# Performance work log

Hardware: AMD Instinct MI355X
Metric: run time of the kernel (lower is better)

The kernel has to match this reference:

```python
import jax, jax.numpy as jnp
import numpy as np

B, T, C, H = 2, 2048, 1024, 16
N = C // H
TM_DIM, TD_DIM = 32, 64
EPS = 1e-5 * 8 ** 2  # GroupNorm eps from the module


def setup_inputs() -> dict:
    key = jax.random.key(0)
    ks = jax.random.split(key, 16)
    nrm = lambda k, shp, s: jax.random.normal(k, shp, dtype=jnp.float32) * s
    uni = lambda k, shp, a: jax.random.uniform(k, shp, jnp.float32, -a, a)
    ddd = (jnp.arange(C, dtype=jnp.float32) / C).reshape(1, 1, C)
    return {
        "x": nrm(ks[0], (B, T, C), 1.0),
        "time_maa_x": 1.0 - ddd ** 0.5,
        "time_maa_w": 1.0 - ddd ** 0.5,
        "time_maa_k": 1.0 - ddd ** 0.5,
        "time_maa_v": 1.0 - (ddd ** 0.5 + 0.15),
        "time_maa_r": 1.0 - ddd ** 0.25,
        "time_maa_g": 1.0 - ddd ** 0.25,
        "time_maa_w1": uni(ks[1], (C, 5 * TM_DIM), 1e-4),
        "time_maa_w2": uni(ks[2], (5, TM_DIM, C), 1e-4),
        "time_decay": jnp.linspace(-6.0, -1.0, C).astype(jnp.float32).reshape(1, 1, C),
        "time_decay_w1": uni(ks[3], (C, TD_DIM), 1e-4),
        "time_decay_w2": uni(ks[4], (TD_DIM, C), 1e-4),
        "time_faaaa": nrm(ks[5], (H, N), 0.1),
        "W_r": nrm(ks[6], (C, C), C ** -0.5),
        "W_k": nrm(ks[7], (C, C), C ** -0.5),
        "W_v": nrm(ks[8], (C, C), C ** -0.5),
        "W_g": nrm(ks[9], (C, C), C ** -0.5),
        "W_o": nrm(ks[10], (C, C), C ** -0.5),
        "ln_w": jnp.ones((C,), jnp.float32),
        "ln_b": jnp.zeros((C,), jnp.float32),
    }


def _forward(x, tmx, tmw, tmk, tmv, tmr, tmg, maa_w1, maa_w2, tdecay, td_w1,
             td_w2, u, Wr, Wk, Wv, Wg, Wo, ln_w, ln_b):
    Bq, Tq, Cq = x.shape
    # time_shift: x[t-1] with zero at t=0
    xx = jnp.concatenate([jnp.zeros_like(x[:, :1]), x[:, :-1]], axis=1) - x
    xxx = x + xx * tmx
    t5 = jnp.tanh(xxx @ maa_w1).reshape(Bq, Tq, 5, TM_DIM)
    m = jnp.einsum('btfe,fec->fbtc', t5, maa_w2)  # [5,B,T,C] data-dependent mix
    xw = x + xx * (tmw + m[0])
    xk = x + xx * (tmk + m[1])
    xv = x + xx * (tmv + m[2])
    xr = x + xx * (tmr + m[3])
    xg = x + xx * (tmg + m[4])
    r = xr @ Wr
    k = xk @ Wk
    v = xv @ Wv
    g = jax.nn.silu(xg @ Wg)
    w = tdecay + jnp.tanh(xw @ td_w1) @ td_w2          # [B,T,C] log-log decay
    decay = jnp.exp(-jnp.exp(w))                        # in (0,1)
    to_tbhn = lambda a: a.reshape(Bq, Tq, H, N).transpose(1, 0, 2, 3)
    rT, kT, vT, dT = (to_tbhn(a) for a in (r, k, v, decay))

    def step(S, inp):  # S: [B,H,N,N] (key_dim i, value_dim j)
        r_t, k_t, v_t, d_t = inp
        kv = k_t[..., :, None] * v_t[..., None, :]
        y = jnp.einsum('bhi,bhij->bhj', r_t, S + u[None, :, :, None] * kv)
        return d_t[..., None] * S + kv, y

    S0 = jnp.zeros((Bq, H, N, N), x.dtype)
    _, ys = jax.lax.scan(step, S0, (rT, kT, vT, dT))
    y = ys.transpose(1, 0, 2, 3).reshape(Bq, Tq, Cq)
    # GroupNorm with H groups over channels
    yh = y.reshape(Bq, Tq, H, N)
    mu = yh.mean(-1, keepdims=True)
    var = yh.var(-1, keepdims=True)
    yn = (yh - mu) / jnp.sqrt(var + EPS)
    yn = (yn * ln_w.reshape(H, N) + ln_b.reshape(H, N)).reshape(Bq, Tq, Cq)
    return (yn * g) @ Wo


def reference(x, time_maa_x, time_maa_w, time_maa_k, time_maa_v, time_maa_r,
              time_maa_g, time_maa_w1, time_maa_w2, time_decay, time_decay_w1,
              time_decay_w2, time_faaaa, W_r, W_k, W_v, W_g, W_o, ln_w, ln_b):
    return _forward(x, time_maa_x, time_maa_w, time_maa_k, time_maa_v,
                    time_maa_r, time_maa_g, time_maa_w1, time_maa_w2,
                    time_decay, time_decay_w1, time_decay_w2, time_faaaa,
                    W_r, W_k, W_v, W_g, W_o, ln_w, ln_b)
```

## Files before the change

### kernel.cpp

```cpp
#include <hip/hip_runtime.h>
#include <hip/hip_bf16.h>
#include <cstdint>
#include <cstddef>

#define B_ 2
#define T_ 2048
#define C_ 1024
#define H_ 16
#define NCH 32
#define CHL 64

typedef unsigned short ushort_t;
typedef __bf16 bf16x8 __attribute__((ext_vector_type(8)));
typedef float f32x4 __attribute__((ext_vector_type(4)));

__device__ __forceinline__ ushort_t f2bf(float f) {
  union { float f; uint32_t u; } x; x.f = f;
  uint32_t r = x.u + 0x7fffu + ((x.u >> 16) & 1u);
  return (ushort_t)(r >> 16);
}
__device__ __forceinline__ float bf2f(ushort_t h) {
  union { uint32_t u; float f; } x; x.u = (uint32_t)h << 16; return x.f;
}

__device__ __forceinline__ void gload16(const void* g, void* l) {
  __builtin_amdgcn_global_load_lds(
      (const __attribute__((address_space(1))) void*)g,
      (__attribute__((address_space(3))) void*)l, 16, 0, 0);
}

__device__ __forceinline__ void stb(ushort_t* tile, int row, int col, ushort_t v) {
  *(ushort_t*)((char*)tile + row * 128 + ((col * 2) ^ ((row & 7) << 4))) = v;
}
__device__ __forceinline__ bf16x8 ldb(const ushort_t* tile, int row, int kbyte) {
  return *(const bf16x8*)((const char*)tile + row * 128 + (kbyte ^ ((row & 7) << 4)));
}

struct TDesc { const float* src; ushort_t* dst; int R, Cc, Cpad; };
struct TArgs { TDesc d[9]; };

__global__ __launch_bounds__(256) void transpose_cvt(TArgs args) {
  TDesc D = args.d[blockIdx.z];
  int c0 = blockIdx.x * 32, r0 = blockIdx.y * 32;
  if (c0 >= D.Cpad || r0 >= D.R) return;
  __shared__ float tile[32][33];
  int tx = threadIdx.x & 31, ty = threadIdx.x >> 5;
#pragma unroll
  for (int i = 0; i < 32; i += 8) {
    int r = r0 + ty + i, c = c0 + tx;
    tile[ty + i][tx] = (r < D.R && c < D.Cc) ? D.src[(size_t)r * D.Cc + c] : 0.f;
  }
  __syncthreads();
#pragma unroll
  for (int i = 0; i < 32; i += 8) {
    int c = c0 + ty + i, r = r0 + tx;
    if (c < D.Cpad && r < D.R) D.dst[(size_t)c * D.R + r] = f2bf(tile[tx][ty + i]);
  }
}

__global__ __launch_bounds__(256) void prep_kernel(
    const float* __restrict__ x, const float* __restrict__ tmx,
    float* __restrict__ xx, ushort_t* __restrict__ xxx) {
  size_t idx = ((size_t)blockIdx.x * 256 + threadIdx.x) * 4;
  int tt = (int)((idx >> 10) & (T_ - 1));
  int c = (int)(idx & (C_ - 1));
  float4 xv = *(const float4*)&x[idx];
  float4 xp;
  if (tt == 0) { xp.x = xp.y = xp.z = xp.w = 0.f; }
  else xp = *(const float4*)&x[idx - C_];
  float4 tm = *(const float4*)&tmx[c];
  float4 d;
  d.x = xp.x - xv.x; d.y = xp.y - xv.y; d.z = xp.z - xv.z; d.w = xp.w - xv.w;
  *(float4*)&xx[idx] = d;
  xxx[idx + 0] = f2bf(xv.x + d.x * tm.x);
  xxx[idx + 1] = f2bf(xv.y + d.y * tm.y);
  xxx[idx + 2] = f2bf(xv.z + d.z * tm.z);
  xxx[idx + 3] = f2bf(xv.w + d.w * tm.w);
}

template <int EPI>
__global__ __launch_bounds__(256) void gemm_bt(
    const ushort_t* __restrict__ A, int lda,
    const ushort_t* __restrict__ Bt, int ldb,
    void* __restrict__ Cp, int ldc, int K,
    const float* __restrict__ aux2) {
  __shared__ ushort_t sA[128 * 32];
  __shared__ ushort_t sB[128 * 32];
  const int t = threadIdx.x;
  const int l = t & 63;
  const int w = t >> 6;
  const int wm = w >> 1, wn = w & 1;
  const int m0 = blockIdx.x * 128, n0 = blockIdx.y * 128;
  const int lr = l & 15;
  const int lk = (l >> 4) * 8;

  f32x4 acc[4][4] = {};

  for (int kt = 0; kt < K; kt += 32) {
    __syncthreads();
#pragma unroll
    for (int it = 0; it < 2; ++it) {
      int cbase = it * 256 + w * 64;
      int ca = cbase + l;
      int row = ca >> 2, kc = ca & 3;
      gload16(A + (size_t)(m0 + row) * lda + kt + kc * 8, (char*)sA + (size_t)cbase * 16);
      gload16(Bt + (size_t)(n0 + row) * ldb + kt + kc * 8, (char*)sB + (size_t)cbase * 16);
    }
    __syncthreads();
    bf16x8 af[4], bfr[4];
#pragma unroll
    for (int mi = 0; mi < 4; ++mi)
      af[mi] = *(const bf16x8*)&sA[(wm * 64 + mi * 16 + lr) * 32 + lk];
#pragma unroll
    for (int ni = 0; ni < 4; ++ni)
      bfr[ni] = *(const bf16x8*)&sB[(wn * 64 + ni * 16 + lr) * 32 + lk];
#pragma unroll
    for (int mi = 0; mi < 4; ++mi)
#pragma unroll
      for (int ni = 0; ni < 4; ++ni)
        acc[mi][ni] = __builtin_amdgcn_mfma_f32_16x16x32_bf16(af[mi], bfr[ni], acc[mi][ni], 0, 0, 0);
  }
#pragma unroll
  for (int mi = 0; mi < 4; ++mi) {
#pragma unroll
    for (int ni = 0; ni < 4; ++ni) {
      int col = n0 + wn * 64 + ni * 16 + lr;
#pragma unroll
      for (int r = 0; r < 4; ++r) {
        int row = m0 + wm * 64 + mi * 16 + (l >> 4) * 4 + r;
        float v = acc[mi][ni][r];
        size_t idx = (size_t)row * ldc + col;
        if constexpr (EPI == 0) {
          ((float*)Cp)[idx] = v;
        } else if constexpr (EPI == 2) {
          ((ushort_t*)Cp)[idx] = f2bf(tanhf(v));
        } else if constexpr (EPI == 4) {
          ((float*)Cp)[idx] = __expf(aux2[col] + v);
        }
      }
    }
  }
}

struct PDesc { const ushort_t* A; const ushort_t* Bt; float* C; int epi; };
struct PArgs { PDesc d[4]; };

__global__ __launch_bounds__(256, 3) void gemm_proj4(PArgs args) {
  PDesc D = args.d[blockIdx.z];
  __shared__ ushort_t sA[128 * 32];
  __shared__ ushort_t sB[128 * 32];
  const int t = threadIdx.x;
  const int l = t & 63;
  const int w = t >> 6;
  const int wm = w >> 1, wn = w & 1;
  const int m0 = blockIdx.x * 128, n0 = blockIdx.y * 128;
  const int lr = l & 15;
  const int lk = (l >> 4) * 8;

  f32x4 acc[4][4] = {};

  for (int kt = 0; kt < C_; kt += 32) {
    __syncthreads();
#pragma unroll
    for (int it = 0; it < 2; ++it) {
      int cbase = it * 256 + w * 64;
      int ca = cbase + l;
      int row = ca >> 2, kc = ca & 3;
      gload16(D.A + (size_t)(m0 + row) * C_ + kt + kc * 8, (char*)sA + (size_t)cbase * 16);
      gload16(D.Bt + (size_t)(n0 + row) * C_ + kt + kc * 8, (char*)sB + (size_t)cbase * 16);
    }
    __syncthreads();
    bf16x8 af[4], bfr[4];
#pragma unroll
    for (int mi = 0; mi < 4; ++mi)
      af[mi] = *(const bf16x8*)&sA[(wm * 64 + mi * 16 + lr) * 32 + lk];
#pragma unroll
    for (int ni = 0; ni < 4; ++ni)
      bfr[ni] = *(const bf16x8*)&sB[(wn * 64 + ni * 16 + lr) * 32 + lk];
#pragma unroll
    for (int mi = 0; mi < 4; ++mi)
#pragma unroll
      for (int ni = 0; ni < 4; ++ni)
        acc[mi][ni] = __builtin_amdgcn_mfma_f32_16x16x32_bf16(af[mi], bfr[ni], acc[mi][ni], 0, 0, 0);
  }
  const int epi = D.epi;
#pragma unroll
  for (int mi = 0; mi < 4; ++mi) {
#pragma unroll
    for (int ni = 0; ni < 4; ++ni) {
      int col = n0 + wn * 64 + ni * 16 + lr;
#pragma unroll
      for (int r = 0; r < 4; ++r) {
        int row = m0 + wm * 64 + mi * 16 + (l >> 4) * 4 + r;
        float v = acc[mi][ni][r];
        if (epi) v = v / (1.f + expf(-v));
        D.C[(size_t)row * C_ + col] = v;
      }
    }
  }
}

struct MixArgs { const float* tm[5]; ushort_t* dst[5]; };

__global__ __launch_bounds__(256) void fused_mix(
    const float* __restrict__ x, const float* __restrict__ xx,
    const ushort_t* __restrict__ t5, const ushort_t* __restrict__ w2t,
    MixArgs margs) {
  __shared__ float xs[64 * 128];
  __shared__ float xxs[64 * 128];
  __shared__ ushort_t sA[64 * 32];
  __shared__ ushort_t sB[128 * 32];
  const int t = threadIdx.x;
  const int l = t & 63;
  const int w = t >> 6;
  const int wm = w >> 1, wn = w & 1;
  const int m0 = blockIdx.x * 64, n0 = blockIdx.y * 128;
  const int lr = l & 15;
  const int lk = (l >> 4) * 8;

#pragma unroll
  for (int it = 0; it < 8; ++it) {
    int row = it * 8 + (t >> 5);
    int c16 = t & 31;
    gload16(x + (size_t)(m0 + row) * C_ + n0 + c16 * 4, (char*)xs + row * 512 + c16 * 16);
    gload16(xx + (size_t)(m0 + row) * C_ + n0 + c16 * 4, (char*)xxs + row * 512 + c16 * 16);
  }

  for (int f = 0; f < 5; ++f) {
    __syncthreads();
    {
      int row = t >> 2, c8 = t & 3;
      gload16(t5 + (size_t)(m0 + row) * 256 + f * 32 + c8 * 8, (char*)sA + t * 16);
    }
#pragma unroll
    for (int it = 0; it < 2; ++it) {
      int row = it * 64 + (t >> 2), c8 = t & 3;
      gload16(w2t + (size_t)(n0 + row) * 160 + f * 32 + c8 * 8,
              (char*)sB + it * 4096 + t * 16);
    }
    __syncthreads();
    bf16x8 af[2], bfr[4];
#pragma unroll
    for (int mi = 0; mi < 2; ++mi)
      af[mi] = *(const bf16x8*)&sA[(wm * 32 + mi * 16 + lr) * 32 + lk];
#pragma unroll
    for (int ni = 0; ni < 4; ++ni)
      bfr[ni] = *(const bf16x8*)&sB[(wn * 64 + ni * 16 + lr) * 32 + lk];
    f32x4 acc[2][4] = {};
#pragma unroll
    for (int mi = 0; mi < 2; ++mi)
#pragma unroll
      for (int ni = 0; ni < 4; ++ni)
        acc[mi][ni] = __builtin_amdgcn_mfma_f32_16x16x32_bf16(af[mi], bfr[ni], acc[mi][ni], 0, 0, 0);
    const float* tmf = margs.tm[f];
    ushort_t* dst = margs.dst[f];
#pragma unroll
    for (int mi = 0; mi < 2; ++mi) {
#pragma unroll
      for (int ni = 0; ni < 4; ++ni) {
        int cl = wn * 64 + ni * 16 + lr;
        int col = n0 + cl;
        float tmv = tmf[col];
#pragma unroll
        for (int r = 0; r < 4; ++r) {
          int rl = wm * 32 + mi * 16 + (l >> 4) * 4 + r;
          int row = m0 + rl;
          float xv = xs[rl * 128 + cl];
          float xxv = xxs[rl * 128 + cl];
          dst[(size_t)row * C_ + col] = f2bf(xv + xxv * (tmv + acc[mi][ni][r]));
        }
      }
    }
  }
}

__global__ __launch_bounds__(256) void chunk_local(
    const float* __restrict__ rx, const float* __restrict__ kx,
    const float* __restrict__ vx, const float* __restrict__ lamx,
    const float* __restrict__ u, float* __restrict__ Mt,
    float* __restrict__ aLg, ushort_t* __restrict__ rAg,
    float* __restrict__ yo) {
  int c = blockIdx.x, bh = blockIdx.y;
  int b = bh >> 4, h = bh & 15;
  __shared__ ushort_t sRA[64 * 64], sKA[64 * 64], sKh[64 * 64], sKl[64 * 64],
                      sVh[64 * 64], sVl[64 * 64], sP[64 * 64];
  __shared__ float qsum[4][64];
  __shared__ float ruk[64];
  const int tid = threadIdx.x;
  const int i = tid & 63;
  const int q = tid >> 6;
  size_t base = ((size_t)b * T_ + (size_t)c * CHL) * C_ + h * 64;
  size_t cb = ((size_t)c * 32 + bh);

  float lam[16];
  float run = 0.f;
#pragma unroll
  for (int s = 0; s < 16; ++s) {
    lam[s] = lamx[base + (size_t)(q * 16 + s) * C_ + i];
    run += lam[s];
  }
  qsum[q][i] = run;
  __syncthreads();
  float pre = 0.f, ct = 0.f;
#pragma unroll
  for (int qq = 0; qq < 4; ++qq) {
    float vq = qsum[qq][i];
    ct += vq;
    if (qq < q) pre += vq;
  }
  float uu = u[h * 64 + i];
  float ci = pre;
#pragma unroll
  for (int s = 0; s < 16; ++s) {
    int t = q * 16 + s;
    ci += lam[s];
    float cl = ci - lam[s];
    size_t o = base + (size_t)t * C_ + i;
    float rv = rx[o], kv = kx[o], vv = vx[o];
    ushort_t ra = f2bf(rv * __expf(-cl));
    stb(sRA, t, i, ra);
    rAg[cb * 4096 + t * 64 + i] = ra;
    stb(sKA, t, i, f2bf(kv * __expf(ci)));
    float kal = kv * __expf(ci - ct);
    ushort_t khv = f2bf(kal);
    stb(sKh, i, t, khv);
    stb(sKl, i, t, f2bf(kal - bf2f(khv)));
    ushort_t vhv = f2bf(vv);
    stb(sVh, i, t, vhv);
    stb(sVl, i, t, f2bf(vv - bf2f(vhv)));
    float rr = rv * uu * kv;
#pragma unroll
    for (int m = 32; m; m >>= 1) rr += __shfl_xor(rr, m);
    if (i == 0) ruk[t] = rr;
  }
  if (q == 0) aLg[cb * 64 + i] = __expf(-ct);
  __syncthreads();

  const int l = tid & 63, w = tid >> 6;
  const int wm = w >> 1, wn = w & 1;
  const int lr = l & 15, hi4 = l >> 4;

  {
    f32x4 accP[2][2] = {};
#pragma unroll
    for (int kk = 0; kk < 2; ++kk) {
      bf16x8 af[2], bf_[2];
#pragma unroll
      for (int mi = 0; mi < 2; ++mi) af[mi] = ldb(sRA, wm * 32 + mi * 16 + lr, kk * 64 + hi4 * 16);
#pragma unroll
      for (int ni = 0; ni < 2; ++ni) bf_[ni] = ldb(sKA, wn * 32 + ni * 16 + lr, kk * 64 + hi4 * 16);
#pragma unroll
      for (int mi = 0; mi < 2; ++mi)
#pragma unroll
        for (int ni = 0; ni < 2; ++ni)
          accP[mi][ni] = __builtin_amdgcn_mfma_f32_16x16x32_bf16(af[mi], bf_[ni], accP[mi][ni], 0, 0, 0);
    }
#pragma unroll
    for (int mi = 0; mi < 2; ++mi)
#pragma unroll
      for (int ni = 0; ni < 2; ++ni)
#pragma unroll
        for (int r = 0; r < 4; ++r) {
          int tl = wm * 32 + mi * 16 + hi4 * 4 + r, sl = wn * 32 + ni * 16 + lr;
          float v = accP[mi][ni][r];
          v = sl < tl ? v : (sl == tl ? ruk[tl] : 0.f);
          stb(sP, tl, sl, f2bf(v));
        }
  }
  __syncthreads();

  f32x4 accY[2][2] = {}, accM[2][2] = {};
#pragma unroll
  for (int kk = 0; kk < 2; ++kk) {
    bf16x8 pa[2], vhA[2], vlA[2], vhB[2], vlB[2], khB[2], klB[2];
#pragma unroll
    for (int mi = 0; mi < 2; ++mi) {
      int rw = wm * 32 + mi * 16 + lr;
      pa[mi] = ldb(sP, rw, kk * 64 + hi4 * 16);
      vhA[mi] = ldb(sVh, rw, kk * 64 + hi4 * 16);
      vlA[mi] = ldb(sVl, rw, kk * 64 + hi4 * 16);
    }
#pragma unroll
    for (int ni = 0; ni < 2; ++ni) {
      int rw = wn * 32 + ni * 16 + lr;
      vhB[ni] = ldb(sVh, rw, kk * 64 + hi4 * 16);
      vlB[ni] = ldb(sVl, rw, kk * 64 + hi4 * 16);
      khB[ni] = ldb(sKh, rw, kk * 64 + hi4 * 16);
      klB[ni] = ldb(sKl, rw, kk * 64 + hi4 * 16);
    }
#pragma unroll
    for (int mi = 0; mi < 2; ++mi)
#pragma unroll
      for (int ni = 0; ni < 2; ++ni) {
        accY[mi][ni] = __builtin_amdgcn_mfma_f32_16x16x32_bf16(pa[mi], vhB[ni], accY[mi][ni], 0, 0, 0);
        accY[mi][ni] = __builtin_amdgcn_mfma_f32_16x16x32_bf16(pa[mi], vlB[ni], accY[mi][ni], 0, 0, 0);
        accM[mi][ni] = __builtin_amdgcn_mfma_f32_16x16x32_bf16(vhA[mi], khB[ni], accM[mi][ni], 0, 0, 0);
        accM[mi][ni] = __builtin_amdgcn_mfma_f32_16x16x32_bf16(vhA[mi], klB[ni], accM[mi][ni], 0, 0, 0);
        accM[mi][ni] = __builtin_amdgcn_mfma_f32_16x16x32_bf16(vlA[mi], khB[ni], accM[mi][ni], 0, 0, 0);
      }
  }
#pragma unroll
  for (int mi = 0; mi < 2; ++mi)
#pragma unroll
    for (int ni = 0; ni < 2; ++ni)
#pragma unroll
      for (int r = 0; r < 4; ++r) {
        int rw = wm * 32 + mi * 16 + hi4 * 4 + r;
        int cw = wn * 32 + ni * 16 + lr;
        yo[base + (size_t)rw * C_ + cw] = accY[mi][ni][r];
        Mt[cb * 4096 + rw * 64 + cw] = accM[mi][ni][r];
      }
}

__global__ __launch_bounds__(256) void combine2(
    const float* __restrict__ Mt, const float* __restrict__ aLg,
    ushort_t* __restrict__ S0h, ushort_t* __restrict__ S0l) {
  int bh = blockIdx.x >> 4;
  int ij = (blockIdx.x & 15) * 256 + threadIdx.x;
  int i = ij & 63;
  float s = 0.f;
  for (int c = 0; c < NCH; ++c) {
    size_t o = ((size_t)c * 32 + bh) * 4096 + ij;
    float m = Mt[o];
    float p = aLg[((size_t)c * 32 + bh) * 64 + i];
    ushort_t hi = f2bf(s);
    S0h[o] = hi;
    S0l[o] = f2bf(s - bf2f(hi));
    s = p * s + m;
  }
}

__global__ __launch_bounds__(256) void inter_gn(
    const ushort_t* __restrict__ rAg, const ushort_t* __restrict__ S0h,
    const ushort_t* __restrict__ S0l, const float* __restrict__ yin,
    const float* __restrict__ gx, const float* __restrict__ lnw,
    const float* __restrict__ lnb, ushort_t* __restrict__ Z) {
  int c = blockIdx.x, bh = blockIdx.y;
  int b = bh >> 4, h = bh & 15;
  __shared__ ushort_t sRA[64 * 64], sSh[64 * 64], sSl[64 * 64];
  __shared__ float st[64][2][2];
  const int tid = threadIdx.x;
  size_t cb = ((size_t)c * 32 + bh) * 4096;
#pragma unroll
  for (int it = 0; it < 2; ++it) {
    int lb = tid * 32 + it * 16;
    int row = lb >> 7, wi = lb & 127;
    int so = row * 128 + (wi ^ ((row & 7) << 4));
    *(uint4*)((char*)sRA + so) = *(const uint4*)((const char*)(rAg + cb) + lb);
    *(uint4*)((char*)sSh + so) = *(const uint4*)((const char*)(S0h + cb) + lb);
    *(uint4*)((char*)sSl + so) = *(const uint4*)((const char*)(S0l + cb) + lb);
  }
  const int l = tid & 63, w = tid >> 6;
  const int wm = w >> 1, wn = w & 1;
  const int lr = l & 15, hi4 = l >> 4;
  size_t base = ((size_t)b * T_ + (size_t)c * CHL) * C_ + h * 64;

  f32x4 acc[2][2];
#pragma unroll
  for (int mi = 0; mi < 2; ++mi)
#pragma unroll
    for (int ni = 0; ni < 2; ++ni)
#pragma unroll
      for (int r = 0; r < 4; ++r)
        acc[mi][ni][r] = yin[base + (size_t)(wm * 32 + mi * 16 + hi4 * 4 + r) * C_ +
                             wn * 32 + ni * 16 + lr];
  __syncthreads();
#pragma unroll
  for (int kk = 0; kk < 2; ++kk) {
    bf16x8 af[2], bh_[2], bl_[2];
#pragma unroll
    for (int mi = 0; mi < 2; ++mi) af[mi] = ldb(sRA, wm * 32 + mi * 16 + lr, kk * 64 + hi4 * 16);
#pragma unroll
    for (int ni = 0; ni < 2; ++ni) {
      bh_[ni] = ldb(sSh, wn * 32 + ni * 16 + lr, kk * 64 + hi4 * 16);
      bl_[ni] = ldb(sSl, wn * 32 + ni * 16 + lr, kk * 64 + hi4 * 16);
    }
#pragma unroll
    for (int mi = 0; mi < 2; ++mi)
#pragma unroll
      for (int ni = 0; ni < 2; ++ni) {
        acc[mi][ni] = __builtin_amdgcn_mfma_f32_16x16x32_bf16(af[mi], bh_[ni], acc[mi][ni], 0, 0, 0);
        acc[mi][ni] = __builtin_amdgcn_mfma_f32_16x16x32_bf16(af[mi], bl_[ni], acc[mi][ni], 0, 0, 0);
      }
  }
#pragma unroll
  for (int mi = 0; mi < 2; ++mi)
#pragma unroll
    for (int r = 0; r < 4; ++r) {
      int row = wm * 32 + mi * 16 + hi4 * 4 + r;
      float s1 = acc[mi][0][r] + acc[mi][1][r];
      float s2 = acc[mi][0][r] * acc[mi][0][r] + acc[mi][1][r] * acc[mi][1][r];
#pragma unroll
      for (int m = 1; m < 16; m <<= 1) { s1 += __shfl_xor(s1, m); s2 += __shfl_xor(s2, m); }
      if (lr == 0) { st[row][wn][0] = s1; st[row][wn][1] = s2; }
    }
  __syncthreads();
#pragma unroll
  for (int mi = 0; mi < 2; ++mi)
#pragma unroll
    for (int ni = 0; ni < 2; ++ni)
#pragma unroll
      for (int r = 0; r < 4; ++r) {
        int row = wm * 32 + mi * 16 + hi4 * 4 + r;
        int jl = wn * 32 + ni * 16 + lr;
        float S1 = st[row][0][0] + st[row][1][0];
        float S2 = st[row][0][1] + st[row][1][1];
        float mu = S1 * (1.f / 64.f);
        float var = S2 * (1.f / 64.f) - mu * mu;
        float rs = rsqrtf(var + 6.4e-4f);
        int col = h * 64 + jl;
        size_t o = base + (size_t)row * C_ + jl;
        float yn = (acc[mi][ni][r] - mu) * rs * lnw[col] + lnb[col];
        Z[o] = f2bf(yn * gx[o]);
      }
}

extern "C" void kernel_launch(void* const* d_in, const int* in_sizes, int n_in,
                              void* d_out, int out_size, void* d_ws, size_t ws_size,
                              hipStream_t stream) {
  const float* x    = (const float*)d_in[0];
  const float* tmx  = (const float*)d_in[1];
  const float* tmw  = (const float*)d_in[2];
  const float* tmk  = (const float*)d_in[3];
  const float* tmv  = (const float*)d_in[4];
  const float* tmr  = (const float*)d_in[5];
  const float* tmg  = (const float*)d_in[6];
  const float* maaw1 = (const float*)d_in[7];
  const float* maaw2 = (const float*)d_in[8];
  const float* tdec = (const float*)d_in[9];
  const float* tdw1 = (const float*)d_in[10];
  const float* tdw2 = (const float*)d_in[11];
  const float* u    = (const float*)d_in[12];
  const float* Wr   = (const float*)d_in[13];
  const float* Wk   = (const float*)d_in[14];
  const float* Wv   = (const float*)d_in[15];
  const float* Wg   = (const float*)d_in[16];
  const float* Wo   = (const float*)d_in[17];
  const float* lnw  = (const float*)d_in[18];
  const float* lnb  = (const float*)d_in[19];

  char* ws = (char*)d_ws;
  const size_t MB = 1ull << 20;
  float*    xx     = (float*)(ws + 0);
  ushort_t* xxx    = (ushort_t*)(ws + 16 * MB);
  ushort_t* WrT    = (ushort_t*)(ws + 24 * MB);
  ushort_t* WkT    = (ushort_t*)(ws + 26 * MB);
  ushort_t* WvT    = (ushort_t*)(ws + 28 * MB);
  ushort_t* WgT    = (ushort_t*)(ws + 30 * MB);
  ushort_t* WoT    = (ushort_t*)(ws + 32 * MB);
  ushort_t* maaW1T = (ushort_t*)(ws + 34 * MB);
  ushort_t* tdW1T  = (ushort_t*)(ws + 35 * MB);
  ushort_t* tdW2T  = (ushort_t*)(ws + 35 * MB + 256 * 1024);
  ushort_t* maaW2T = (ushort_t*)(ws + 35 * MB + 512 * 1024);
  ushort_t* t5     = (ushort_t*)(ws + 36 * MB);
  ushort_t* t5d    = (ushort_t*)(ws + 38 * MB);
  ushort_t* Xm[5];
  for (int f = 0; f < 5; ++f) Xm[f] = (ushort_t*)(ws + 40 * MB + (size_t)f * 8 * MB);
  float*    Mtb = (float*)(ws + 40 * MB);
  ushort_t* S0h = (ushort_t*)(ws + 56 * MB);
  ushort_t* S0l = (ushort_t*)(ws + 64 * MB);
  ushort_t* rAg = (ushort_t*)(ws + 72 * MB);
  float* rb   = (float*)(ws + 80 * MB);
  float* kb   = (float*)(ws + 96 * MB);
  float* vb   = (float*)(ws + 112 * MB);
  float* gb   = (float*)(ws + 128 * MB);
  float* lam  = (float*)(ws + 144 * MB);
  float* aLg  = (float*)(ws + 160 * MB);
  float* yb   = (float*)(ws + 0);
  ushort_t* Zb = (ushort_t*)(ws + 16 * MB);

  TArgs ta;
  ta.d[0] = TDesc{Wr,    WrT,    1024, 1024, 1024};
  ta.d[1] = TDesc{Wk,    WkT,    1024, 1024, 1024};
  ta.d[2] = TDesc{Wv,    WvT,    1024, 1024, 1024};
  ta.d[3] = TDesc{Wg,    WgT,    1024, 1024, 1024};
  ta.d[4] = TDesc{Wo,    WoT,    1024, 1024, 1024};
  ta.d[5] = TDesc{maaw1, maaW1T, 1024, 160,  256};
  ta.d[6] = TDesc{tdw1,  tdW1T,  1024, 64,   128};
  ta.d[7] = TDesc{tdw2,  tdW2T,  64,   1024, 1024};
  ta.d[8] = TDesc{maaw2, maaW2T, 160,  1024, 1024};
  transpose_cvt<<<dim3(32, 32, 9), 256, 0, stream>>>(ta);

  prep_kernel<<<(B_ * T_ * C_) / 1024, 256, 0, stream>>>(x, tmx, xx, xxx);

  gemm_bt<2><<<dim3(32, 2), 256, 0, stream>>>(xxx, C_, maaW1T, C_, t5, 256, C_, nullptr);

  MixArgs ma;
  ma.tm[0] = tmw; ma.tm[1] = tmk; ma.tm[2] = tmv; ma.tm[3] = tmr; ma.tm[4] = tmg;
  for (int f = 0; f < 5; ++f) ma.dst[f] = Xm[f];
  fused_mix<<<dim3(64, 8), 256, 0, stream>>>(x, xx, t5, maaW2T, ma);

  PArgs pa;
  pa.d[0] = PDesc{Xm[3], WrT, rb, 0};
  pa.d[1] = PDesc{Xm[1], WkT, kb, 0};
  pa.d[2] = PDesc{Xm[2], WvT, vb, 0};
  pa.d[3] = PDesc{Xm[4], WgT, gb, 1};
  gemm_proj4<<<dim3(32, 8, 4), 256, 0, stream>>>(pa);

  gemm_bt<2><<<dim3(32, 1), 256, 0, stream>>>(Xm[0], C_, tdW1T, C_, t5d, 128, C_, nullptr);
  gemm_bt<4><<<dim3(32, 8), 256, 0, stream>>>(t5d, 128, tdW2T, 64, lam, C_, 64, tdec);

  chunk_local<<<dim3(NCH, B_ * H_), 256, 0, stream>>>(rb, kb, vb, lam, u, Mtb, aLg, rAg, yb);
  combine2<<<512, 256, 0, stream>>>(Mtb, aLg, S0h, S0l);
  inter_gn<<<dim3(NCH, B_ * H_), 256, 0, stream>>>(rAg, S0h, S0l, yb, gb, lnw, lnb, Zb);

  gemm_bt<0><<<dim3(32, 8), 256, 0, stream>>>(Zb, C_, WoT, C_, (float*)d_out, C_, C_, nullptr);
}
```

Baseline: 230.8 us.

## Use 256x256 double-buffered projection GEMM, smaller-tile tanh GEMM, vectorized combine

The four-way r/k/v/g projection GEMM now uses 256x256 tiles, 512 threads, swizzled LDS, double-buffered async global-to-LDS loads with explicit vmcnt waits, and setprio around the MFMAs. This raises data reuse per tile and overlaps loads with compute. The small tanh-epilogue GEMMs use a new 64-row tile kernel to launch more blocks. The combine scan now handles four floats per thread with vector loads and stores. Risks: the larger tiles give only 256 blocks, which may underfill the GPU, and the higher register/LDS use limits occupancy.

```diff
diff --git a/kernel.cpp b/kernel.cpp
--- a/kernel.cpp
+++ b/kernel.cpp
@@ -28,6 +28,9 @@
       (const __attribute__((address_space(1))) void*)g,
       (__attribute__((address_space(3))) void*)l, 16, 0, 0);
 }
+
+#define FENCE() asm volatile("" ::: "memory")
+#define BAR() do { FENCE(); __builtin_amdgcn_s_barrier(); FENCE(); } while (0)
 
 __device__ __forceinline__ void stb(ushort_t* tile, int row, int col, ushort_t v) {
   *(ushort_t*)((char*)tile + row * 128 + ((col * 2) ^ ((row & 7) << 4))) = v;
@@ -132,8 +135,6 @@
         size_t idx = (size_t)row * ldc + col;
         if constexpr (EPI == 0) {
           ((float*)Cp)[idx] = v;
-        } else if constexpr (EPI == 2) {
-          ((ushort_t*)Cp)[idx] = f2bf(tanhf(v));
         } else if constexpr (EPI == 4) {
           ((float*)Cp)[idx] = __expf(aux2[col] + v);
         }
@@ -142,62 +143,150 @@
   }
 }
 
-struct PDesc { const ushort_t* A; const ushort_t* Bt; float* C; int epi; };
-struct PArgs { PDesc d[4]; };
-
-__global__ __launch_bounds__(256, 3) void gemm_proj4(PArgs args) {
-  PDesc D = args.d[blockIdx.z];
-  __shared__ ushort_t sA[128 * 32];
+__global__ __launch_bounds__(256) void gemm_bt64(
+    const ushort_t* __restrict__ A, int lda,
+    const ushort_t* __restrict__ Bt, int ldb,
+    ushort_t* __restrict__ Cp, int ldc, int K) {
+  __shared__ ushort_t sA[64 * 32];
   __shared__ ushort_t sB[128 * 32];
   const int t = threadIdx.x;
   const int l = t & 63;
   const int w = t >> 6;
-  const int wm = w >> 1, wn = w & 1;
-  const int m0 = blockIdx.x * 128, n0 = blockIdx.y * 128;
-  const int lr = l & 15;
-  const int lk = (l >> 4) * 8;
-
-  f32x4 acc[4][4] = {};
-
-  for (int kt = 0; kt < C_; kt += 32) {
+  const int m0 = blockIdx.x * 64, n0 = blockIdx.y * 128;
+  const int lr = l & 15, lk = (l >> 4) * 8;
+
+  f32x4 acc[4][2] = {};
+  for (int kt = 0; kt < K; kt += 32) {
     __syncthreads();
+    {
+      int row = t >> 2, kc = t & 3;
+      gload16(A + (size_t)(m0 + row) * lda + kt + kc * 8, (char*)sA + w * 1024);
+    }
 #pragma unroll
     for (int it = 0; it < 2; ++it) {
-      int cbase = it * 256 + w * 64;
-      int ca = cbase + l;
+      int ca = it * 256 + t;
       int row = ca >> 2, kc = ca & 3;
-      gload16(D.A + (size_t)(m0 + row) * C_ + kt + kc * 8, (char*)sA + (size_t)cbase * 16);
-      gload16(D.Bt + (size_t)(n0 + row) * C_ + kt + kc * 8, (char*)sB + (size_t)cbase * 16);
+      gload16(Bt + (size_t)(n0 + row) * ldb + kt + kc * 8,
+              (char*)sB + it * 4096 + w * 1024);
     }
     __syncthreads();
-    bf16x8 af[4], bfr[4];
+    bf16x8 af[4], bfr[2];
 #pragma unroll
     for (int mi = 0; mi < 4; ++mi)
-      af[mi] = *(const bf16x8*)&sA[(wm * 64 + mi * 16 + lr) * 32 + lk];
-#pragma unroll
-    for (int ni = 0; ni < 4; ++ni)
-      bfr[ni] = *(const bf16x8*)&sB[(wn * 64 + ni * 16 + lr) * 32 + lk];
+      af[mi] = *(const bf16x8*)&sA[(mi * 16 + lr) * 32 + lk];
+#pragma unroll
+    for (int ni = 0; ni < 2; ++ni)
+      bfr[ni] = *(const bf16x8*)&sB[(w * 32 + ni * 16 + lr) * 32 + lk];
 #pragma unroll
     for (int mi = 0; mi < 4; ++mi)
 #pragma unroll
-      for (int ni = 0; ni < 4; ++ni)
+      for (int ni = 0; ni < 2; ++ni)
         acc[mi][ni] = __builtin_amdgcn_mfma_f32_16x16x32_bf16(af[mi], bfr[ni], acc[mi][ni], 0, 0, 0);
   }
+#pragma unroll
+  for (int mi = 0; mi < 4; ++mi)
+#pragma unroll
+    for (int ni = 0; ni < 2; ++ni) {
+      int col = n0 + w * 32 + ni * 16 + lr;
+#pragma unroll
+      for (int r = 0; r < 4; ++r) {
+        int row = m0 + mi * 16 + (l >> 4) * 4 + r;
+        Cp[(size_t)row * ldc + col] = f2bf(tanhf(acc[mi][ni][r]));
+      }
+    }
+}
+
+struct PDesc { const ushort_t* A; const ushort_t* Bt; float* C; int epi; };
+struct PArgs { PDesc d[4]; };
+
+__device__ __forceinline__ bf16x8 ldsw(const ushort_t* t_, int row, int slot) {
+  return *(const bf16x8*)((const char*)t_ + row * 128 + (((slot ^ (row & 7)) << 4)));
+}
+
+__global__ __launch_bounds__(512, 2) void gemm_proj256(PArgs args) {
+  PDesc D = args.d[blockIdx.z];
+  __shared__ ushort_t sA0[256 * 64], sB0[256 * 64], sA1[256 * 64], sB1[256 * 64];
+  const int tid = threadIdx.x;
+  const int w = tid >> 6, l = tid & 63;
+  const int wm = w >> 2, wn = w & 3;
+  const int lr = l & 15, hi4 = l >> 4;
+  const int m0 = blockIdx.x * 256, n0 = blockIdx.y * 256;
+
+  const int srow = tid >> 3;
+  const int scol = ((tid & 7) ^ (srow & 7)) << 3;
+  const ushort_t* Ag = D.A + (size_t)(m0 + srow) * C_ + scol;
+  const ushort_t* Bg = D.Bt + (size_t)(n0 + srow) * C_ + scol;
+  const int wb = w * 1024;
+
+  f32x4 acc[8][4] = {};
+
+#define STAGE256(sa, sb, kt)                                        \
+  do {                                                              \
+    const ushort_t* ap_ = Ag + (kt);                                \
+    const ushort_t* bp_ = Bg + (kt);                                \
+    gload16(ap_,            (char*)(sa) + 0 * 8192 + wb);           \
+    gload16(ap_ +  64 * C_, (char*)(sa) + 1 * 8192 + wb);           \
+    gload16(ap_ + 128 * C_, (char*)(sa) + 2 * 8192 + wb);           \
+    gload16(ap_ + 192 * C_, (char*)(sa) + 3 * 8192 + wb);           \
+    gload16(bp_,            (char*)(sb) + 0 * 8192 + wb);           \
+    gload16(bp_ +  64 * C_, (char*)(sb) + 1 * 8192 + wb);           \
+    gload16(bp_ + 128 * C_, (char*)(sb) + 2 * 8192 + wb);           \
+    gload16(bp_ + 192 * C_, (char*)(sb) + 3 * 8192 + wb);           \
+  } while (0)
+
+#define KSTEP256(CA, CB, t)                                                  \
+  do {                                                                       \
+    if ((t) < 15) asm volatile("s_waitcnt vmcnt(8)" ::: "memory");           \
+    else          asm volatile("s_waitcnt vmcnt(0)" ::: "memory");           \
+    BAR();                                                                   \
+    _Pragma("unroll")                                                        \
+    for (int kk = 0; kk < 2; ++kk) {                                         \
+      bf16x8 bfrag[4];                                                       \
+      _Pragma("unroll")                                                      \
+      for (int ni = 0; ni < 4; ++ni)                                         \
+        bfrag[ni] = ldsw(CB, wn * 64 + ni * 16 + lr, kk * 4 + hi4);          \
+      __builtin_amdgcn_s_setprio(1);                                         \
+      _Pragma("unroll")                                                      \
+      for (int mi = 0; mi < 8; ++mi) {                                       \
+        bf16x8 af = ldsw(CA, wm * 128 + mi * 16 + lr, kk * 4 + hi4);         \
+        _Pragma("unroll")                                                    \
+        for (int ni = 0; ni < 4; ++ni)                                       \
+          acc[mi][ni] = __builtin_amdgcn_mfma_f32_16x16x32_bf16(             \
+              af, bfrag[ni], acc[mi][ni], 0, 0, 0);                          \
+      }                                                                      \
+      __builtin_amdgcn_s_setprio(0);                                         \
+    }                                                                        \
+    asm volatile("s_waitcnt lgkmcnt(0)" ::: "memory");                       \
+    __builtin_amdgcn_sched_barrier(0);                                       \
+    BAR();                                                                   \
+    if ((t) < 14) STAGE256(CA, CB, ((t) + 2) * 64);                          \
+  } while (0)
+
+  STAGE256(sA0, sB0, 0);
+  STAGE256(sA1, sB1, 64);
+
+#pragma unroll 1
+  for (int tt = 0; tt < 8; ++tt) {
+    KSTEP256(sA0, sB0, tt * 2);
+    KSTEP256(sA1, sB1, tt * 2 + 1);
+  }
+
   const int epi = D.epi;
 #pragma unroll
-  for (int mi = 0; mi < 4; ++mi) {
+  for (int mi = 0; mi < 8; ++mi)
 #pragma unroll
     for (int ni = 0; ni < 4; ++ni) {
       int col = n0 + wn * 64 + ni * 16 + lr;
 #pragma unroll
       for (int r = 0; r < 4; ++r) {
-        int row = m0 + wm * 64 + mi * 16 + (l >> 4) * 4 + r;
+        int row = m0 + wm * 128 + mi * 16 + hi4 * 4 + r;
         float v = acc[mi][ni][r];
-        if (epi) v = v / (1.f + expf(-v));
+        if (epi) v = v / (1.f + __expf(-v));
         D.C[(size_t)row * C_ + col] = v;
       }
     }
-  }
+#undef KSTEP256
+#undef STAGE256
 }
 
 struct MixArgs { const float* tm[5]; ushort_t* dst[5]; };
@@ -415,18 +504,23 @@
 __global__ __launch_bounds__(256) void combine2(
     const float* __restrict__ Mt, const float* __restrict__ aLg,
     ushort_t* __restrict__ S0h, ushort_t* __restrict__ S0l) {
-  int bh = blockIdx.x >> 4;
-  int ij = (blockIdx.x & 15) * 256 + threadIdx.x;
+  int bh = blockIdx.x >> 2;
+  int ij = ((blockIdx.x & 3) * 256 + threadIdx.x) * 4;
   int i = ij & 63;
-  float s = 0.f;
+  float4 s = {0.f, 0.f, 0.f, 0.f};
   for (int c = 0; c < NCH; ++c) {
     size_t o = ((size_t)c * 32 + bh) * 4096 + ij;
-    float m = Mt[o];
-    float p = aLg[((size_t)c * 32 + bh) * 64 + i];
-    ushort_t hi = f2bf(s);
-    S0h[o] = hi;
-    S0l[o] = f2bf(s - bf2f(hi));
-    s = p * s + m;
+    float4 m = *(const float4*)&Mt[o];
+    float4 p = *(const float4*)&aLg[((size_t)c * 32 + bh) * 64 + i];
+    ushort4 hi, lo;
+    hi.x = f2bf(s.x); lo.x = f2bf(s.x - bf2f(hi.x));
+    hi.y = f2bf(s.y); lo.y = f2bf(s.y - bf2f(hi.y));
+    hi.z = f2bf(s.z); lo.z = f2bf(s.z - bf2f(hi.z));
+    hi.w = f2bf(s.w); lo.w = f2bf(s.w - bf2f(hi.w));
+    *(ushort4*)&S0h[o] = hi;
+    *(ushort4*)&S0l[o] = lo;
+    s.x = p.x * s.x + m.x; s.y = p.y * s.y + m.y;
+    s.z = p.z * s.z + m.z; s.w = p.w * s.w + m.w;
   }
 }
 
@@ -583,7 +677,7 @@
 
   prep_kernel<<<(B_ * T_ * C_) / 1024, 256, 0, stream>>>(x, tmx, xx, xxx);
 
-  gemm_bt<2><<<dim3(32, 2), 256, 0, stream>>>(xxx, C_, maaW1T, C_, t5, 256, C_, nullptr);
+  gemm_bt64<<<dim3(64, 2), 256, 0, stream>>>(xxx, C_, maaW1T, C_, t5, 256, C_);
 
   MixArgs ma;
   ma.tm[0] = tmw; ma.tm[1] = tmk; ma.tm[2] = tmv; ma.tm[3] = tmr; ma.tm[4] = tmg;
@@ -595,13 +689,13 @@
   pa.d[1] = PDesc{Xm[1], WkT, kb, 0};
   pa.d[2] = PDesc{Xm[2], WvT, vb, 0};
   pa.d[3] = PDesc{Xm[4], WgT, gb, 1};
-  gemm_proj4<<<dim3(32, 8, 4), 256, 0, stream>>>(pa);
-
-  gemm_bt<2><<<dim3(32, 1), 256, 0, stream>>>(Xm[0], C_, tdW1T, C_, t5d, 128, C_, nullptr);
+  gemm_proj256<<<dim3(16, 4, 4), 512, 0, stream>>>(pa);
+
+  gemm_bt64<<<dim3(64, 1), 256, 0, stream>>>(Xm[0], C_, tdW1T, C_, t5d, 128, C_);
   gemm_bt<4><<<dim3(32, 8), 256, 0, stream>>>(t5d, 128, tdW2T, 64, lam, C_, 64, tdec);
 
   chunk_local<<<dim3(NCH, B_ * H_), 256, 0, stream>>>(rb, kb, vb, lam, u, Mtb, aLg, rAg, yb);
-  combine2<<<512, 256, 0, stream>>>(Mtb, aLg, S0h, S0l);
+  combine2<<<128, 256, 0, stream>>>(Mtb, aLg, S0h, S0l);
   inter_gn<<<dim3(NCH, B_ * H_), 256, 0, stream>>>(rAg, S0h, S0l, yb, gb, lnw, lnb, Zb);
 
   gemm_bt<0><<<dim3(32, 8), 256, 0, stream>>>(Zb, C_, WoT, C_, (float*)d_out, C_, C_, nullptr);
```

Measured after the change: 210.9 us. -8.6%, faster.
